# Optimization experiments

Hardware: AMD Instinct MI355X
Metric: run time of the kernel (lower is better)

Reference implementation:

```python
import jax, jax.numpy as jnp
import numpy as np
from jax import lax

B, S, H = 64, 128, 64
EPS = 1e-5


def _conv1d(x, w, b):
    # x: [B, Cin, S], w: [Cout, Cin, 3], padding=1
    y = lax.conv_general_dilated(x, w, window_strides=(1,), padding=[(1, 1)],
                                 dimension_numbers=("NCH", "OIH", "NCH"))
    return y + b[None, :, None]


def _bn(x, g, b, m, v):
    # eval-mode BatchNorm1d over channel dim of [B, C, S]
    inv = g / jnp.sqrt(v + EPS)
    return x * inv[None, :, None] + (b - m * inv)[None, :, None]


def setup_inputs() -> dict:
    key = jax.random.key(0)
    ks = jax.random.split(key, 24)
    d = {}
    d["x"] = jax.random.normal(ks[0], (B, S, 1), dtype=jnp.float32)
    sc = 0.1
    d["conv1_w"] = jax.random.normal(ks[1], (H, 1, 3), dtype=jnp.float32) * sc
    d["conv1_b"] = jax.random.normal(ks[2], (H,), dtype=jnp.float32) * sc
    d["bn1_g"] = jax.random.uniform(ks[3], (H,), dtype=jnp.float32) + 0.5
    d["bn1_b"] = jax.random.normal(ks[4], (H,), dtype=jnp.float32) * sc
    d["bn1_m"] = jax.random.normal(ks[5], (H,), dtype=jnp.float32) * sc
    d["bn1_v"] = jax.random.uniform(ks[6], (H,), dtype=jnp.float32) + 0.5
    d["conv2_w"] = jax.random.normal(ks[7], (H, H, 3), dtype=jnp.float32) * 0.05
    d["conv2_b"] = jax.random.normal(ks[8], (H,), dtype=jnp.float32) * sc
    d["bn2_g"] = jax.random.uniform(ks[9], (H,), dtype=jnp.float32) + 0.5
    d["bn2_b"] = jax.random.normal(ks[10], (H,), dtype=jnp.float32) * sc
    d["bn2_m"] = jax.random.normal(ks[11], (H,), dtype=jnp.float32) * sc
    d["bn2_v"] = jax.random.uniform(ks[12], (H,), dtype=jnp.float32) + 0.5
    d["gat_W"] = jax.random.normal(ks[13], (H, H), dtype=jnp.float32) * 0.05
    d["gat_Wb"] = jax.random.normal(ks[14], (H,), dtype=jnp.float32) * sc
    d["gat_a1"] = jax.random.normal(ks[15], (H,), dtype=jnp.float32) * sc
    d["gat_a2"] = jax.random.normal(ks[16], (H,), dtype=jnp.float32) * sc
    d["gat_ab"] = jax.random.normal(ks[17], (), dtype=jnp.float32) * sc
    d["ta_W"] = jax.random.normal(ks[18], (H, H), dtype=jnp.float32) * 0.05
    d["ta_b"] = jax.random.normal(ks[19], (H,), dtype=jnp.float32) * sc
    d["p1_W"] = jax.random.normal(ks[20], (32, H), dtype=jnp.float32) * sc
    d["p1_b"] = jax.random.normal(ks[21], (32,), dtype=jnp.float32) * sc
    d["p2_W"] = jax.random.normal(ks[22], (1, 32), dtype=jnp.float32) * sc
    d["p2_b"] = jax.random.normal(ks[23], (1,), dtype=jnp.float32) * sc
    return d


def reference(x, conv1_w, conv1_b, bn1_g, bn1_b, bn1_m, bn1_v,
              conv2_w, conv2_b, bn2_g, bn2_b, bn2_m, bn2_v,
              gat_W, gat_Wb, gat_a1, gat_a2, gat_ab,
              ta_W, ta_b, p1_W, p1_b, p2_W, p2_b):
    b, s, _ = x.shape
    # feature extraction: [B, 1, S] -> [B, H, S]
    h = jnp.transpose(x, (0, 2, 1))
    h = jax.nn.relu(_bn(_conv1d(h, conv1_w, conv1_b), bn1_g, bn1_b, bn1_m, bn1_v))
    h = jax.nn.relu(_bn(_conv1d(h, conv2_w, conv2_b), bn2_g, bn2_b, bn2_m, bn2_v))
    # flatten to N = B*S nodes of dim H
    xf = jnp.transpose(h, (0, 2, 1)).reshape(b * s, H)  # [N, H]
    # dense adjacency: softmax(xf xf^T) over rows (single chunk since B<=100)
    adj = jax.nn.softmax(xf @ xf.T, axis=1)  # [N, N]
    # GAT layer; pairwise score decomposed: a([Wh_i;Wh_j]) = Wh_i.a1 + Wh_j.a2 + b
    Wh = xf @ gat_W.T + gat_Wb  # [N, H]
    s1 = Wh @ gat_a1  # [N]
    s2 = Wh @ gat_a2  # [N]
    e = jax.nn.leaky_relu(s1[:, None] + s2[None, :] + gat_ab, 0.2)  # [N, N]
    e = jnp.where(adj > 0, e, jnp.float32(-9e15))
    att = jax.nn.softmax(e, axis=1)
    hp = att @ Wh  # [N, H]
    h2 = hp.reshape(b, s, H)
    # time attention over feature dim
    tw = jax.nn.softmax(h2 @ ta_W.T + ta_b, axis=2)
    h2 = h2 * tw
    # global average pool over sequence
    pooled = jnp.mean(h2, axis=1)  # [B, H]
    out = jax.nn.relu(pooled @ p1_W.T + p1_b) @ p2_W.T + p2_b  # [B, 1]
    return out
```

## Files before the change

### kernel.cpp

```cpp
#include <hip/hip_runtime.h>
#include <hip/hip_bf16.h>

#define Hd 64
#define Sd 128
#define Bd 64
#define Nn 8192
#define EPSd 1e-5f

__device__ __forceinline__ float wred_sum(float v) {
    for (int m = 32; m; m >>= 1) v += __shfl_xor(v, m);
    return v;
}
__device__ __forceinline__ float wred_max(float v) {
    for (int m = 32; m; m >>= 1) v = fmaxf(v, __shfl_xor(v, m));
    return v;
}
__device__ __forceinline__ float wscan_incl(float x, int lane) {
    #pragma unroll
    for (int d = 1; d < 64; d <<= 1) {
        float t = __shfl_up(x, d);
        if (lane >= d) x += t;
    }
    return x;
}

__global__ __launch_bounds__(256) void kA_feat_wh(
        const float* __restrict__ x,
        const float* __restrict__ c1w, const float* __restrict__ c1b,
        const float* __restrict__ b1g, const float* __restrict__ b1b,
        const float* __restrict__ b1m, const float* __restrict__ b1v,
        const float* __restrict__ c2w, const float* __restrict__ c2b,
        const float* __restrict__ b2g, const float* __restrict__ b2b,
        const float* __restrict__ b2m, const float* __restrict__ b2v,
        const float* __restrict__ gW, const float* __restrict__ gWb,
        const float* __restrict__ a1, const float* __restrict__ a2,
        float* __restrict__ Wh, float* __restrict__ s1, float* __restrict__ s2) {
    __shared__ float buf[14464];
    float* h1  = buf;
    float* wtk = buf + 2176;
    int b  = blockIdx.x >> 2;
    int s0 = (blockIdx.x & 3) * 32;
    int tid = threadIdx.x;
    for (int idx = tid; idx < 12288; idx += 256) {
        int j    = idx & 3;
        int c    = (idx >> 2) & 63;
        int cin4 = (idx >> 8) & 15;
        int k    = idx >> 12;
        wtk[idx] = c2w[(c * 64 + cin4 * 4 + j) * 3 + k];
    }
    for (int idx = tid; idx < 34 * 64; idx += 256) {
        int cin = idx & 63;
        int col = idx >> 6;
        int s   = s0 - 1 + col;
        float v = 0.f;
        if (s >= 0 && s < Sd) {
            float xm = (s > 0)      ? x[b * Sd + s - 1] : 0.f;
            float x0 = x[b * Sd + s];
            float xp = (s < Sd - 1) ? x[b * Sd + s + 1] : 0.f;
            float y  = c1w[cin * 3 + 0] * xm + c1w[cin * 3 + 1] * x0 + c1w[cin * 3 + 2] * xp + c1b[cin];
            float inv = b1g[cin] * rsqrtf(b1v[cin] + EPSd);
            v = fmaxf(y * inv + (b1b[cin] - b1m[cin] * inv), 0.f);
        }
        h1[col * 64 + cin] = v;
    }
    __syncthreads();
    int c = tid & 63, g = tid >> 6;
    float inv2 = b2g[c] * rsqrtf(b2v[c] + EPSd);
    float sh2  = b2b[c] - b2m[c] * inv2;
    float acc[8];
    #pragma unroll
    for (int p = 0; p < 8; ++p) acc[p] = c2b[c];
    {
        const float4* h14 = (const float4*)h1;
        const float4* wt4 = (const float4*)wtk;
        for (int cin4 = 0; cin4 < 16; ++cin4) {
            float4 xs[10];
            #pragma unroll
            for (int q = 0; q < 10; ++q) xs[q] = h14[(g * 8 + q) * 16 + cin4];
            #pragma unroll
            for (int k = 0; k < 3; ++k) {
                float4 w4 = wt4[(k * 16 + cin4) * 64 + c];
                #pragma unroll
                for (int p = 0; p < 8; ++p) {
                    float4 x4 = xs[p + k];
                    acc[p] += w4.x * x4.x + w4.y * x4.y + w4.z * x4.z + w4.w * x4.w;
                }
            }
        }
    }
    __syncthreads();
    float*  xfl  = buf;
    float4* gWT4 = (float4*)(buf + 2176);
    #pragma unroll
    for (int p = 0; p < 8; ++p)
        xfl[(g * 8 + p) * 64 + c] = fmaxf(acc[p] * inv2 + sh2, 0.f);
    for (int fidx = tid; fidx < 1024; fidx += 256) {
        int h_ = fidx >> 4, kk4 = fidx & 15;
        gWT4[kk4 * 64 + h_] = ((const float4*)gW)[fidx];
    }
    __syncthreads();
    int h = tid & 63, w = tid >> 6;
    float4 wreg[16];
    #pragma unroll
    for (int kk4 = 0; kk4 < 16; ++kk4) wreg[kk4] = gWT4[kk4 * 64 + h];
    float va1 = a1[h], va2 = a2[h], bias = gWb[h];
    const float4* xf4 = (const float4*)xfl;
    int n0 = b * Sd + s0;
    for (int q = 0; q < 8; ++q) {
        int sl = w * 8 + q;
        float accw = bias;
        #pragma unroll
        for (int kk4 = 0; kk4 < 16; ++kk4) {
            float4 x4 = xf4[sl * 16 + kk4];
            accw += wreg[kk4].x * x4.x + wreg[kk4].y * x4.y + wreg[kk4].z * x4.z + wreg[kk4].w * x4.w;
        }
        int n = n0 + sl;
        Wh[n * 64 + h] = accw;
        float r1 = wred_sum(accw * va1);
        float r2 = wred_sum(accw * va2);
        if (h == 0) { s1[n] = r1; s2[n] = r2; }
    }
}

__global__ __launch_bounds__(256) void kB_rank(
        const float* __restrict__ s2, const float* __restrict__ s1,
        const float* __restrict__ gab,
        int* __restrict__ rankPart, int* __restrict__ kPart,
        float* __restrict__ pmax) {
    __shared__ float4 ts4[64];
    int bid = blockIdx.x;
    int jg = bid >> 5, part = bid & 31;
    int tid = threadIdx.x;
    if (tid < 64) ts4[tid] = ((const float4*)(s2 + part * 256))[tid];
    __syncthreads();
    if (jg == 0 && tid < 64) {
        float4 t4 = ts4[tid];
        float m = fmaxf(fmaxf(t4.x, t4.y), fmaxf(t4.z, t4.w));
        m = wred_max(m);
        if (tid == 0) pmax[part] = m;
    }
    int j = jg * 256 + tid;
    float tj = s2[j];
    float negc = -(s1[j] + gab[0]);
    int jloc = j - part * 256;
    int cntR = 0, cntK = 0;
    #pragma unroll 4
    for (int q = 0; q < 64; ++q) {
        float4 t4 = ts4[q];
        int rb = q * 4;
        cntR += (t4.x < tj || (t4.x == tj && rb     < jloc)) ? 1 : 0;
        cntR += (t4.y < tj || (t4.y == tj && rb + 1 < jloc)) ? 1 : 0;
        cntR += (t4.z < tj || (t4.z == tj && rb + 2 < jloc)) ? 1 : 0;
        cntR += (t4.w < tj || (t4.w == tj && rb + 3 < jloc)) ? 1 : 0;
        cntK += (t4.x <= negc) ? 1 : 0;
        cntK += (t4.y <= negc) ? 1 : 0;
        cntK += (t4.z <= negc) ? 1 : 0;
        cntK += (t4.w <= negc) ? 1 : 0;
    }
    rankPart[part * 8192 + j] = cntR;
    kPart[part * 8192 + j]    = cntK;
}

__global__ __launch_bounds__(256) void kC_scatter(
        const float* __restrict__ Wh, const float* __restrict__ s2,
        const int* __restrict__ rankPart, const int* __restrict__ kPart,
        float* __restrict__ Rpos, float* __restrict__ Rneg,
        float* __restrict__ spos, float* __restrict__ sneg,
        int* __restrict__ kk) {
    __shared__ int rsl[512], ksl[512];
    __shared__ int rsum[16], ksum[16];
    int tid = threadIdx.x;
    int j0 = blockIdx.x * 16;
    for (int idx = tid; idx < 512; idx += 256) {
        int p = idx >> 4, jj = idx & 15;
        rsl[idx] = rankPart[p * 8192 + j0 + jj];
        ksl[idx] = kPart[p * 8192 + j0 + jj];
    }
    __syncthreads();
    if (tid < 16) {
        int a = 0, bq = 0;
        #pragma unroll
        for (int p = 0; p < 32; ++p) { a += rsl[p * 16 + tid]; bq += ksl[p * 16 + tid]; }
        rsum[tid] = a; ksum[tid] = bq;
    }
    __syncthreads();
    int jj = tid >> 4, h4 = tid & 15;
    int j = j0 + jj;
    int r = rsum[jj];
    float t = s2[j];
    float e1 = expf(t), e2 = expf(0.2f * t);
    float4 wv = ((const float4*)Wh)[j * 16 + h4];
    ((float4*)Rpos)[r * 16 + h4] = make_float4(e1 * wv.x, e1 * wv.y, e1 * wv.z, e1 * wv.w);
    ((float4*)Rneg)[r * 16 + h4] = make_float4(e2 * wv.x, e2 * wv.y, e2 * wv.z, e2 * wv.w);
    if (h4 == 0) { spos[r] = e1; sneg[r] = e2; kk[j] = ksum[jj]; }
}

__global__ __launch_bounds__(256) void kD_csum(
        const float* __restrict__ Rpos, const float* __restrict__ Rneg,
        const float* __restrict__ spos, const float* __restrict__ sneg,
        float* __restrict__ csP, float* __restrict__ csN,
        float* __restrict__ csp, float* __restrict__ csn) {
    __shared__ float ldsP[4][64], ldsN[4][64];
    int ch = blockIdx.x, tid = threadIdx.x;
    int h = tid & 63, w = tid >> 6;
    int rb = ch * 128 + w * 32;
    double aP = 0.0, aN = 0.0;
    #pragma unroll
    for (int r = 0; r < 32; ++r) {
        aP += Rpos[(rb + r) * 64 + h];
        aN += Rneg[(rb + r) * 64 + h];
    }
    ldsP[w][h] = (float)aP; ldsN[w][h] = (float)aN;
    __syncthreads();
    if (w == 0) {
        csP[ch * 64 + h] = ldsP[0][h] + ldsP[1][h] + ldsP[2][h] + ldsP[3][h];
    } else if (w == 1) {
        csN[ch * 64 + h] = ldsN[0][h] + ldsN[1][h] + ldsN[2][h] + ldsN[3][h];
    } else if (w == 2) {
        float v = spos[ch * 128 + h] + spos[ch * 128 + 64 + h];
        v = wred_sum(v);
        if (h == 0) csp[ch] = v;
    } else {
        float v = sneg[ch * 128 + h] + sneg[ch * 128 + 64 + h];
        v = wred_sum(v);
        if (h == 0) csn[ch] = v;
    }
}

__global__ __launch_bounds__(256) void kE_expand(
        const float* __restrict__ Rpos, const float* __restrict__ Rneg,
        const float* __restrict__ spos, const float* __restrict__ sneg,
        const float* __restrict__ csP, const float* __restrict__ csN,
        const float* __restrict__ csp, const float* __restrict__ csn,
        float* __restrict__ Ppos, float* __restrict__ Pneg,
        float* __restrict__ ppos, float* __restrict__ pneg) {
    __shared__ float ldsA[4][64], ldsB[4][64];
    __shared__ float cbPs[64], cbNs[64];
    int ch = blockIdx.x, tid = threadIdx.x;
    int h = tid & 63, w = tid >> 6;
    double bp = 0.0, bn = 0.0;
    for (int p = w; p < ch; p += 4) { bp += csP[p * 64 + h]; bn += csN[p * 64 + h]; }
    ldsA[w][h] = (float)bp; ldsB[w][h] = (float)bn;
    __syncthreads();
    if (w == 0) {
        cbPs[h] = ldsA[0][h] + ldsA[1][h] + ldsA[2][h] + ldsA[3][h];
        cbNs[h] = ldsB[0][h] + ldsB[1][h] + ldsB[2][h] + ldsB[3][h];
    }
    __syncthreads();
    float cbP = cbPs[h], cbN = cbNs[h];
    int rb = ch * 128 + w * 32;
    float v[32];
    #pragma unroll
    for (int r = 0; r < 32; ++r) v[r] = Rpos[(rb + r) * 64 + h];
    double acc = 0.0;
    #pragma unroll
    for (int r = 0; r < 32; ++r) acc += v[r];
    ldsA[w][h] = (float)acc;
    __syncthreads();
    float off = cbP;
    #pragma unroll
    for (int w2 = 0; w2 < 4; ++w2) if (w2 < w) off += ldsA[w2][h];
    double a2_ = 0.0;
    #pragma unroll
    for (int r = 0; r < 32; ++r) { Ppos[(rb + r) * 64 + h] = off + (float)a2_; a2_ += v[r]; }
    if (ch == 63 && w == 3) Ppos[Nn * 64 + h] = off + (float)a2_;
    __syncthreads();
    #pragma unroll
    for (int r = 0; r < 32; ++r) v[r] = Rneg[(rb + r) * 64 + h];
    acc = 0.0;
    #pragma unroll
    for (int r = 0; r < 32; ++r) acc += v[r];
    ldsB[w][h] = (float)acc;
    __syncthreads();
    off = cbN;
    #pragma unroll
    for (int w2 = 0; w2 < 4; ++w2) if (w2 < w) off += ldsB[w2][h];
    a2_ = 0.0;
    #pragma unroll
    for (int r = 0; r < 32; ++r) { Pneg[(rb + r) * 64 + h] = off + (float)a2_; a2_ += v[r]; }
    if (ch == 63 && w == 3) Pneg[Nn * 64 + h] = off + (float)a2_;
    if (w == 0) {
        int lane = h;
        float bs = (lane < ch) ? csp[lane] : 0.f;
        bs = wred_sum(bs);
        float v0 = spos[ch * 128 + lane], v1 = spos[ch * 128 + 64 + lane];
        float i0 = wscan_incl(v0, lane);
        float t0 = __shfl(i0, 63);
        float i1 = wscan_incl(v1, lane);
        ppos[ch * 128 + lane]      = bs + i0 - v0;
        ppos[ch * 128 + 64 + lane] = bs + t0 + i1 - v1;
        if (ch == 63 && lane == 63) ppos[Nn] = bs + t0 + i1;
    } else if (w == 1) {
        int lane = h;
        float bs = (lane < ch) ? csn[lane] : 0.f;
        bs = wred_sum(bs);
        float v0 = sneg[ch * 128 + lane], v1 = sneg[ch * 128 + 64 + lane];
        float i0 = wscan_incl(v0, lane);
        float t0 = __shfl(i0, 63);
        float i1 = wscan_incl(v1, lane);
        pneg[ch * 128 + lane]      = bs + i0 - v0;
        pneg[ch * 128 + 64 + lane] = bs + t0 + i1 - v1;
        if (ch == 63 && lane == 63) pneg[Nn] = bs + t0 + i1;
    }
}

__global__ __launch_bounds__(256) void kF_node(
        const float* __restrict__ s1, const int* __restrict__ kk,
        const float* __restrict__ pmax, const float* __restrict__ gab,
        const float* __restrict__ Ppos, const float* __restrict__ Pneg,
        const float* __restrict__ ppos, const float* __restrict__ pneg,
        const float* __restrict__ taW, const float* __restrict__ tab,
        float* __restrict__ h2) {
    __shared__ float4 wt4[1024];
    __shared__ float hl[16 * 64];
    int tid = threadIdx.x;
    for (int fidx = tid; fidx < 1024; fidx += 256) {
        int h_ = fidx >> 4, kk4 = fidx & 15;
        wt4[kk4 * 64 + h_] = ((const float4*)taW)[fidx];
    }
    float tmx = pmax[tid & 31];
    tmx = wred_max(tmx);
    __syncthreads();
    int h = tid & 63, w = tid >> 6;
    float gabv = gab[0];
    float tabv = tab[h];
    float Tp  = Ppos[Nn * 64 + h];
    float ppT = ppos[Nn];
    for (int r = 0; r < 4; ++r) {
        int n = blockIdx.x * 16 + w * 4 + r;
        float c = s1[n] + gabv;
        int k = kk[n];
        float z = c + tmx;
        float m = (z >= 0.f) ? z : 0.2f * z;
        float E1 = expf(c - m), E2 = expf(0.2f * c - m);
        float Pp = Ppos[k * 64 + h], Pn = Pneg[k * 64 + h];
        float num = E1 * (Tp - Pp) + E2 * Pn;
        float den = E1 * (ppT - ppos[k]) + E2 * pneg[k];
        float hp = num / den;
        int slot = w * 4 + r;
        hl[slot * 64 + h] = hp;
        float vv = tabv;
        const float4* hlr = (const float4*)&hl[slot * 64];
        #pragma unroll
        for (int kk4 = 0; kk4 < 16; ++kk4) {
            float4 w4 = wt4[kk4 * 64 + h];
            float4 x4 = hlr[kk4];
            vv += w4.x * x4.x + w4.y * x4.y + w4.z * x4.z + w4.w * x4.w;
        }
        float mx = wred_max(vv);
        float e = expf(vv - mx);
        float se = wred_sum(e);
        h2[n * 64 + h] = hp * (e / se);
    }
}

__global__ __launch_bounds__(256) void kG_pool(
        const float* __restrict__ h2,
        const float* __restrict__ p1W, const float* __restrict__ p1b,
        const float* __restrict__ p2W, const float* __restrict__ p2b,
        float* __restrict__ out) {
    __shared__ float pacc[4 * 64];
    __shared__ float pl[64];
    __shared__ float p1s[32 * 65];
    int tid = threadIdx.x, b = blockIdx.x;
    int w = tid >> 6, h = tid & 63;
    for (int idx = tid; idx < 2048; idx += 256) {
        int q = idx >> 6, kq = idx & 63;
        p1s[q * 65 + kq] = p1W[idx];
    }
    float a = 0.f;
    for (int s = w * 32; s < w * 32 + 32; ++s) a += h2[(b * Sd + s) * 64 + h];
    pacc[w * 64 + h] = a;
    __syncthreads();
    if (w == 0) {
        float pooled = (pacc[h] + pacc[64 + h] + pacc[128 + h] + pacc[192 + h]) * (1.f / 128.f);
        pl[h] = pooled;
        float val = 0.f;
        if (h < 32) {
            float acc = p1b[h];
            #pragma unroll
            for (int kq = 0; kq < 64; ++kq) acc += p1s[h * 65 + kq] * pl[kq];
            val = p2W[h] * fmaxf(acc, 0.f);
        }
        val = wred_sum(val);
        if (h == 0) out[b] = val + p2b[0];
    }
}

extern "C" void kernel_launch(void* const* d_in, const int* in_sizes, int n_in,
                              void* d_out, int out_size, void* d_ws, size_t ws_size,
                              hipStream_t stream) {
    const float* x    = (const float*)d_in[0];
    const float* c1w  = (const float*)d_in[1];
    const float* c1b  = (const float*)d_in[2];
    const float* b1g  = (const float*)d_in[3];
    const float* b1b  = (const float*)d_in[4];
    const float* b1m  = (const float*)d_in[5];
    const float* b1v  = (const float*)d_in[6];
    const float* c2w  = (const float*)d_in[7];
    const float* c2b  = (const float*)d_in[8];
    const float* b2g  = (const float*)d_in[9];
    const float* b2b  = (const float*)d_in[10];
    const float* b2m  = (const float*)d_in[11];
    const float* b2v  = (const float*)d_in[12];
    const float* gW   = (const float*)d_in[13];
    const float* gWb  = (const float*)d_in[14];
    const float* ga1  = (const float*)d_in[15];
    const float* ga2  = (const float*)d_in[16];
    const float* gab  = (const float*)d_in[17];
    const float* taW  = (const float*)d_in[18];
    const float* tab  = (const float*)d_in[19];
    const float* p1W  = (const float*)d_in[20];
    const float* p1b  = (const float*)d_in[21];
    const float* p2W  = (const float*)d_in[22];
    const float* p2b  = (const float*)d_in[23];
    float* out = (float*)d_out;

    float* ws = (float*)d_ws;
    float* Wh      = ws;
    float* s1      = Wh + 524288;
    float* s2v     = s1 + 8192;
    float* spos    = s2v + 8192;
    float* sneg    = spos + 8192;
    float* ppos    = sneg + 8192;
    float* pneg    = ppos + 8256;
    float* csP     = pneg + 8256;
    float* csN     = csP + 4096;
    float* csp     = csN + 4096;
    float* csn     = csp + 64;
    float* pmax    = csn + 64;
    int*   kk      = (int*)(pmax + 64);
    int*   rankPart= kk + 8192;
    int*   kPart   = rankPart + 262144;
    float* Rpos    = (float*)(kPart + 262144);
    float* Rneg    = Rpos + 524288;
    float* Ppos    = Rneg + 524288;
    float* Pneg    = Ppos + 524352;
    float* h2      = Rpos;

    kA_feat_wh<<<256, 256, 0, stream>>>(x, c1w, c1b, b1g, b1b, b1m, b1v,
                                        c2w, c2b, b2g, b2b, b2m, b2v,
                                        gW, gWb, ga1, ga2, Wh, s1, s2v);
    kB_rank<<<1024, 256, 0, stream>>>(s2v, s1, gab, rankPart, kPart, pmax);
    kC_scatter<<<512, 256, 0, stream>>>(Wh, s2v, rankPart, kPart,
                                        Rpos, Rneg, spos, sneg, kk);
    kD_csum<<<64, 256, 0, stream>>>(Rpos, Rneg, spos, sneg, csP, csN, csp, csn);
    kE_expand<<<64, 256, 0, stream>>>(Rpos, Rneg, spos, sneg, csP, csN, csp, csn,
                                      Ppos, Pneg, ppos, pneg);
    kF_node<<<512, 256, 0, stream>>>(s1, kk, pmax, gab, Ppos, Pneg, ppos, pneg,
                                     taW, tab, h2);
    kG_pool<<<64, 256, 0, stream>>>(h2, p1W, p1b, p2W, p2b, out);
}
```

Measured before the change: 68.57 us.

## Fuse scatter/cumsum/expand and node/pool kernels with inter-block flag barriers

```diff
diff --git a/kernel.cpp b/kernel.cpp
--- a/kernel.cpp
+++ b/kernel.cpp
@@ -35,11 +35,11 @@
         const float* __restrict__ gW, const float* __restrict__ gWb,
         const float* __restrict__ a1, const float* __restrict__ a2,
         float* __restrict__ Wh, float* __restrict__ s1, float* __restrict__ s2) {
-    __shared__ float buf[14464];
+    __shared__ float buf[13440];
     float* h1  = buf;
-    float* wtk = buf + 2176;
-    int b  = blockIdx.x >> 2;
-    int s0 = (blockIdx.x & 3) * 32;
+    float* wtk = buf + 1152;
+    int b  = blockIdx.x >> 3;
+    int s0 = (blockIdx.x & 7) * 16;
     int tid = threadIdx.x;
     for (int idx = tid; idx < 12288; idx += 256) {
         int j    = idx & 3;
@@ -48,7 +48,7 @@
         int k    = idx >> 12;
         wtk[idx] = c2w[(c * 64 + cin4 * 4 + j) * 3 + k];
     }
-    for (int idx = tid; idx < 34 * 64; idx += 256) {
+    for (int idx = tid; idx < 1152; idx += 256) {
         int cin = idx & 63;
         int col = idx >> 6;
         int s   = s0 - 1 + col;
@@ -67,21 +67,21 @@
     int c = tid & 63, g = tid >> 6;
     float inv2 = b2g[c] * rsqrtf(b2v[c] + EPSd);
     float sh2  = b2b[c] - b2m[c] * inv2;
-    float acc[8];
-    #pragma unroll
-    for (int p = 0; p < 8; ++p) acc[p] = c2b[c];
+    float acc[4];
+    #pragma unroll
+    for (int p = 0; p < 4; ++p) acc[p] = c2b[c];
     {
         const float4* h14 = (const float4*)h1;
         const float4* wt4 = (const float4*)wtk;
         for (int cin4 = 0; cin4 < 16; ++cin4) {
-            float4 xs[10];
+            float4 xs[6];
             #pragma unroll
-            for (int q = 0; q < 10; ++q) xs[q] = h14[(g * 8 + q) * 16 + cin4];
+            for (int q = 0; q < 6; ++q) xs[q] = h14[(g * 4 + q) * 16 + cin4];
             #pragma unroll
             for (int k = 0; k < 3; ++k) {
                 float4 w4 = wt4[(k * 16 + cin4) * 64 + c];
                 #pragma unroll
-                for (int p = 0; p < 8; ++p) {
+                for (int p = 0; p < 4; ++p) {
                     float4 x4 = xs[p + k];
                     acc[p] += w4.x * x4.x + w4.y * x4.y + w4.z * x4.z + w4.w * x4.w;
                 }
@@ -90,10 +90,10 @@
     }
     __syncthreads();
     float*  xfl  = buf;
-    float4* gWT4 = (float4*)(buf + 2176);
-    #pragma unroll
-    for (int p = 0; p < 8; ++p)
-        xfl[(g * 8 + p) * 64 + c] = fmaxf(acc[p] * inv2 + sh2, 0.f);
+    float4* gWT4 = (float4*)(buf + 1152);
+    #pragma unroll
+    for (int p = 0; p < 4; ++p)
+        xfl[(g * 4 + p) * 64 + c] = fmaxf(acc[p] * inv2 + sh2, 0.f);
     for (int fidx = tid; fidx < 1024; fidx += 256) {
         int h_ = fidx >> 4, kk4 = fidx & 15;
         gWT4[kk4 * 64 + h_] = ((const float4*)gW)[fidx];
@@ -106,8 +106,8 @@
     float va1 = a1[h], va2 = a2[h], bias = gWb[h];
     const float4* xf4 = (const float4*)xfl;
     int n0 = b * Sd + s0;
-    for (int q = 0; q < 8; ++q) {
-        int sl = w * 8 + q;
+    for (int q = 0; q < 4; ++q) {
+        int sl = w * 4 + q;
         float accw = bias;
         #pragma unroll
         for (int kk4 = 0; kk4 < 16; ++kk4) {
@@ -126,11 +126,14 @@
         const float* __restrict__ s2, const float* __restrict__ s1,
         const float* __restrict__ gab,
         int* __restrict__ rankPart, int* __restrict__ kPart,
-        float* __restrict__ pmax) {
+        float* __restrict__ pmax, int* __restrict__ flagsZ) {
     __shared__ float4 ts4[64];
     int bid = blockIdx.x;
     int jg = bid >> 5, part = bid & 31;
     int tid = threadIdx.x;
+    if (bid == 0) {
+        for (int i = tid; i < 640; i += 256) flagsZ[i] = 0;
+    }
     if (tid < 64) ts4[tid] = ((const float4*)(s2 + part * 256))[tid];
     __syncthreads();
     if (jg == 0 && tid < 64) {
@@ -161,83 +164,85 @@
     kPart[part * 8192 + j]    = cntK;
 }
 
-__global__ __launch_bounds__(256) void kC_scatter(
+__global__ __launch_bounds__(256) void kCDE(
         const float* __restrict__ Wh, const float* __restrict__ s2,
         const int* __restrict__ rankPart, const int* __restrict__ kPart,
         float* __restrict__ Rpos, float* __restrict__ Rneg,
         float* __restrict__ spos, float* __restrict__ sneg,
-        int* __restrict__ kk) {
-    __shared__ int rsl[512], ksl[512];
-    __shared__ int rsum[16], ksum[16];
-    int tid = threadIdx.x;
-    int j0 = blockIdx.x * 16;
-    for (int idx = tid; idx < 512; idx += 256) {
-        int p = idx >> 4, jj = idx & 15;
+        int* __restrict__ kk,
+        float* __restrict__ csP, float* __restrict__ csN,
+        float* __restrict__ csp, float* __restrict__ csn,
+        float* __restrict__ Ppos, float* __restrict__ Pneg,
+        float* __restrict__ ppos, float* __restrict__ pneg,
+        int* __restrict__ flag1, int* __restrict__ flag2) {
+    __shared__ int rsl[4096], ksl[4096];
+    __shared__ float e1s[128], e2s[128];
+    __shared__ int rj[128];
+    __shared__ float ldsA[4][64], ldsB[4][64], cbPs[64], cbNs[64];
+    int ch = blockIdx.x, tid = threadIdx.x;
+    int j0 = ch * 128;
+    for (int idx = tid; idx < 4096; idx += 256) {
+        int p = idx >> 7, jj = idx & 127;
         rsl[idx] = rankPart[p * 8192 + j0 + jj];
         ksl[idx] = kPart[p * 8192 + j0 + jj];
     }
     __syncthreads();
-    if (tid < 16) {
-        int a = 0, bq = 0;
+    if (tid < 128) {
+        int r = 0, kq = 0;
         #pragma unroll
-        for (int p = 0; p < 32; ++p) { a += rsl[p * 16 + tid]; bq += ksl[p * 16 + tid]; }
-        rsum[tid] = a; ksum[tid] = bq;
-    }
-    __syncthreads();
-    int jj = tid >> 4, h4 = tid & 15;
-    int j = j0 + jj;
-    int r = rsum[jj];
-    float t = s2[j];
-    float e1 = expf(t), e2 = expf(0.2f * t);
-    float4 wv = ((const float4*)Wh)[j * 16 + h4];
-    ((float4*)Rpos)[r * 16 + h4] = make_float4(e1 * wv.x, e1 * wv.y, e1 * wv.z, e1 * wv.w);
-    ((float4*)Rneg)[r * 16 + h4] = make_float4(e2 * wv.x, e2 * wv.y, e2 * wv.z, e2 * wv.w);
-    if (h4 == 0) { spos[r] = e1; sneg[r] = e2; kk[j] = ksum[jj]; }
-}
-
-__global__ __launch_bounds__(256) void kD_csum(
-        const float* __restrict__ Rpos, const float* __restrict__ Rneg,
-        const float* __restrict__ spos, const float* __restrict__ sneg,
-        float* __restrict__ csP, float* __restrict__ csN,
-        float* __restrict__ csp, float* __restrict__ csn) {
-    __shared__ float ldsP[4][64], ldsN[4][64];
-    int ch = blockIdx.x, tid = threadIdx.x;
+        for (int p = 0; p < 32; ++p) { r += rsl[p * 128 + tid]; kq += ksl[p * 128 + tid]; }
+        rj[tid] = r;
+        float t = s2[j0 + tid];
+        float e1 = expf(t), e2 = expf(0.2f * t);
+        e1s[tid] = e1; e2s[tid] = e2;
+        spos[r] = e1; sneg[r] = e2;
+        kk[j0 + tid] = kq;
+    }
+    __syncthreads();
+    for (int it = tid; it < 2048; it += 256) {
+        int jj = it >> 4, h4 = it & 15;
+        int r = rj[jj];
+        float4 wv = ((const float4*)Wh)[(j0 + jj) * 16 + h4];
+        float e1 = e1s[jj], e2 = e2s[jj];
+        ((float4*)Rpos)[r * 16 + h4] = make_float4(e1 * wv.x, e1 * wv.y, e1 * wv.z, e1 * wv.w);
+        ((float4*)Rneg)[r * 16 + h4] = make_float4(e2 * wv.x, e2 * wv.y, e2 * wv.z, e2 * wv.w);
+    }
+    __threadfence();
+    __syncthreads();
+    if (tid == 0) atomicExch(&flag1[ch], 1);
+    if (tid < 64) { while (atomicAdd(&flag1[tid], 0) == 0) __builtin_amdgcn_s_sleep(2); }
+    __syncthreads();
+    __threadfence();
     int h = tid & 63, w = tid >> 6;
     int rb = ch * 128 + w * 32;
-    double aP = 0.0, aN = 0.0;
-    #pragma unroll
-    for (int r = 0; r < 32; ++r) {
-        aP += Rpos[(rb + r) * 64 + h];
-        aN += Rneg[(rb + r) * 64 + h];
-    }
-    ldsP[w][h] = (float)aP; ldsN[w][h] = (float)aN;
+    float v[32], u[32];
+    #pragma unroll
+    for (int r = 0; r < 32; ++r) { v[r] = Rpos[(rb + r) * 64 + h]; u[r] = Rneg[(rb + r) * 64 + h]; }
+    double sP = 0.0, sN = 0.0;
+    #pragma unroll
+    for (int r = 0; r < 32; ++r) { sP += v[r]; sN += u[r]; }
+    float sPf = (float)sP, sNf = (float)sN;
+    ldsA[w][h] = sPf; ldsB[w][h] = sNf;
     __syncthreads();
     if (w == 0) {
-        csP[ch * 64 + h] = ldsP[0][h] + ldsP[1][h] + ldsP[2][h] + ldsP[3][h];
+        csP[ch * 64 + h] = ldsA[0][h] + ldsA[1][h] + ldsA[2][h] + ldsA[3][h];
     } else if (w == 1) {
-        csN[ch * 64 + h] = ldsN[0][h] + ldsN[1][h] + ldsN[2][h] + ldsN[3][h];
+        csN[ch * 64 + h] = ldsB[0][h] + ldsB[1][h] + ldsB[2][h] + ldsB[3][h];
     } else if (w == 2) {
-        float v = spos[ch * 128 + h] + spos[ch * 128 + 64 + h];
-        v = wred_sum(v);
-        if (h == 0) csp[ch] = v;
+        float vv = spos[ch * 128 + h] + spos[ch * 128 + 64 + h];
+        vv = wred_sum(vv);
+        if (h == 0) csp[ch] = vv;
     } else {
-        float v = sneg[ch * 128 + h] + sneg[ch * 128 + 64 + h];
-        v = wred_sum(v);
-        if (h == 0) csn[ch] = v;
-    }
-}
-
-__global__ __launch_bounds__(256) void kE_expand(
-        const float* __restrict__ Rpos, const float* __restrict__ Rneg,
-        const float* __restrict__ spos, const float* __restrict__ sneg,
-        const float* __restrict__ csP, const float* __restrict__ csN,
-        const float* __restrict__ csp, const float* __restrict__ csn,
-        float* __restrict__ Ppos, float* __restrict__ Pneg,
-        float* __restrict__ ppos, float* __restrict__ pneg) {
-    __shared__ float ldsA[4][64], ldsB[4][64];
-    __shared__ float cbPs[64], cbNs[64];
-    int ch = blockIdx.x, tid = threadIdx.x;
-    int h = tid & 63, w = tid >> 6;
+        float vv = sneg[ch * 128 + h] + sneg[ch * 128 + 64 + h];
+        vv = wred_sum(vv);
+        if (h == 0) csn[ch] = vv;
+    }
+    __threadfence();
+    __syncthreads();
+    if (tid == 0) atomicExch(&flag2[ch], 1);
+    if (tid < 64) { while (atomicAdd(&flag2[tid], 0) == 0) __builtin_amdgcn_s_sleep(2); }
+    __syncthreads();
+    __threadfence();
     double bp = 0.0, bn = 0.0;
     for (int p = w; p < ch; p += 4) { bp += csP[p * 64 + h]; bn += csN[p * 64 + h]; }
     ldsA[w][h] = (float)bp; ldsB[w][h] = (float)bn;
@@ -247,38 +252,19 @@
         cbNs[h] = ldsB[0][h] + ldsB[1][h] + ldsB[2][h] + ldsB[3][h];
     }
     __syncthreads();
-    float cbP = cbPs[h], cbN = cbNs[h];
-    int rb = ch * 128 + w * 32;
-    float v[32];
-    #pragma unroll
-    for (int r = 0; r < 32; ++r) v[r] = Rpos[(rb + r) * 64 + h];
-    double acc = 0.0;
-    #pragma unroll
-    for (int r = 0; r < 32; ++r) acc += v[r];
-    ldsA[w][h] = (float)acc;
-    __syncthreads();
-    float off = cbP;
-    #pragma unroll
-    for (int w2 = 0; w2 < 4; ++w2) if (w2 < w) off += ldsA[w2][h];
-    double a2_ = 0.0;
-    #pragma unroll
-    for (int r = 0; r < 32; ++r) { Ppos[(rb + r) * 64 + h] = off + (float)a2_; a2_ += v[r]; }
-    if (ch == 63 && w == 3) Ppos[Nn * 64 + h] = off + (float)a2_;
-    __syncthreads();
-    #pragma unroll
-    for (int r = 0; r < 32; ++r) v[r] = Rneg[(rb + r) * 64 + h];
-    acc = 0.0;
-    #pragma unroll
-    for (int r = 0; r < 32; ++r) acc += v[r];
-    ldsB[w][h] = (float)acc;
-    __syncthreads();
-    off = cbN;
-    #pragma unroll
-    for (int w2 = 0; w2 < 4; ++w2) if (w2 < w) off += ldsB[w2][h];
-    a2_ = 0.0;
-    #pragma unroll
-    for (int r = 0; r < 32; ++r) { Pneg[(rb + r) * 64 + h] = off + (float)a2_; a2_ += v[r]; }
-    if (ch == 63 && w == 3) Pneg[Nn * 64 + h] = off + (float)a2_;
+    ldsA[w][h] = sPf; ldsB[w][h] = sNf;
+    __syncthreads();
+    float offP = cbPs[h], offN = cbNs[h];
+    #pragma unroll
+    for (int w2 = 0; w2 < 4; ++w2) if (w2 < w) { offP += ldsA[w2][h]; offN += ldsB[w2][h]; }
+    double a = 0.0;
+    #pragma unroll
+    for (int r = 0; r < 32; ++r) { Ppos[(rb + r) * 64 + h] = offP + (float)a; a += v[r]; }
+    if (ch == 63 && w == 3) Ppos[Nn * 64 + h] = offP + (float)a;
+    a = 0.0;
+    #pragma unroll
+    for (int r = 0; r < 32; ++r) { Pneg[(rb + r) * 64 + h] = offN + (float)a; a += u[r]; }
+    if (ch == 63 && w == 3) Pneg[Nn * 64 + h] = offN + (float)a;
     if (w == 0) {
         int lane = h;
         float bs = (lane < ch) ? csp[lane] : 0.f;
@@ -304,16 +290,22 @@
     }
 }
 
-__global__ __launch_bounds__(256) void kF_node(
+__global__ __launch_bounds__(256) void kFG(
         const float* __restrict__ s1, const int* __restrict__ kk,
         const float* __restrict__ pmax, const float* __restrict__ gab,
         const float* __restrict__ Ppos, const float* __restrict__ Pneg,
         const float* __restrict__ ppos, const float* __restrict__ pneg,
         const float* __restrict__ taW, const float* __restrict__ tab,
-        float* __restrict__ h2) {
+        const float* __restrict__ p1W, const float* __restrict__ p1b,
+        const float* __restrict__ p2W, const float* __restrict__ p2b,
+        float* __restrict__ h2, float* __restrict__ out,
+        int* __restrict__ flagF) {
     __shared__ float4 wt4[1024];
     __shared__ float hl[16 * 64];
-    int tid = threadIdx.x;
+    __shared__ float pacc[4 * 64];
+    __shared__ float pl[64];
+    __shared__ float p1s[32 * 65];
+    int tid = threadIdx.x, bid = blockIdx.x;
     for (int fidx = tid; fidx < 1024; fidx += 256) {
         int h_ = fidx >> 4, kk4 = fidx & 15;
         wt4[kk4 * 64 + h_] = ((const float4*)taW)[fidx];
@@ -327,7 +319,7 @@
     float Tp  = Ppos[Nn * 64 + h];
     float ppT = ppos[Nn];
     for (int r = 0; r < 4; ++r) {
-        int n = blockIdx.x * 16 + w * 4 + r;
+        int n = bid * 16 + w * 4 + r;
         float c = s1[n] + gabv;
         int k = kk[n];
         float z = c + tmx;
@@ -352,18 +344,14 @@
         float se = wred_sum(e);
         h2[n * 64 + h] = hp * (e / se);
     }
-}
-
-__global__ __launch_bounds__(256) void kG_pool(
-        const float* __restrict__ h2,
-        const float* __restrict__ p1W, const float* __restrict__ p1b,
-        const float* __restrict__ p2W, const float* __restrict__ p2b,
-        float* __restrict__ out) {
-    __shared__ float pacc[4 * 64];
-    __shared__ float pl[64];
-    __shared__ float p1s[32 * 65];
-    int tid = threadIdx.x, b = blockIdx.x;
-    int w = tid >> 6, h = tid & 63;
+    __threadfence();
+    __syncthreads();
+    if (tid == 0) atomicExch(&flagF[bid], 1);
+    if (bid & 7) return;
+    int b = bid >> 3;
+    if (tid < 8) { while (atomicAdd(&flagF[bid + tid], 0) == 0) __builtin_amdgcn_s_sleep(2); }
+    __syncthreads();
+    __threadfence();
     for (int idx = tid; idx < 2048; idx += 256) {
         int q = idx >> 6, kq = idx & 63;
         p1s[q * 65 + kq] = p1W[idx];
@@ -429,7 +417,11 @@
     float* csp     = csN + 4096;
     float* csn     = csp + 64;
     float* pmax    = csn + 64;
-    int*   kk      = (int*)(pmax + 64);
+    int*   flags   = (int*)(pmax + 64);
+    int*   flag1   = flags;
+    int*   flag2   = flags + 64;
+    int*   flagF   = flags + 128;
+    int*   kk      = flags + 640;
     int*   rankPart= kk + 8192;
     int*   kPart   = rankPart + 262144;
     float* Rpos    = (float*)(kPart + 262144);
@@ -438,16 +430,14 @@
     float* Pneg    = Ppos + 524352;
     float* h2      = Rpos;
 
-    kA_feat_wh<<<256, 256, 0, stream>>>(x, c1w, c1b, b1g, b1b, b1m, b1v,
+    kA_feat_wh<<<512, 256, 0, stream>>>(x, c1w, c1b, b1g, b1b, b1m, b1v,
                                         c2w, c2b, b2g, b2b, b2m, b2v,
                                         gW, gWb, ga1, ga2, Wh, s1, s2v);
-    kB_rank<<<1024, 256, 0, stream>>>(s2v, s1, gab, rankPart, kPart, pmax);
-    kC_scatter<<<512, 256, 0, stream>>>(Wh, s2v, rankPart, kPart,
-                                        Rpos, Rneg, spos, sneg, kk);
-    kD_csum<<<64, 256, 0, stream>>>(Rpos, Rneg, spos, sneg, csP, csN, csp, csn);
-    kE_expand<<<64, 256, 0, stream>>>(Rpos, Rneg, spos, sneg, csP, csN, csp, csn,
-                                      Ppos, Pneg, ppos, pneg);
-    kF_node<<<512, 256, 0, stream>>>(s1, kk, pmax, gab, Ppos, Pneg, ppos, pneg,
-                                     taW, tab, h2);
-    kG_pool<<<64, 256, 0, stream>>>(h2, p1W, p1b, p2W, p2b, out);
-}
+    kB_rank<<<1024, 256, 0, stream>>>(s2v, s1, gab, rankPart, kPart, pmax, flags);
+    kCDE<<<64, 256, 0, stream>>>(Wh, s2v, rankPart, kPart,
+                                 Rpos, Rneg, spos, sneg, kk,
+                                 csP, csN, csp, csn,
+                                 Ppos, Pneg, ppos, pneg, flag1, flag2);
+    kFG<<<512, 256, 0, stream>>>(s1, kk, pmax, gab, Ppos, Pneg, ppos, pneg,
+                                 taW, tab, p1W, p1b, p2W, p2b, h2, out, flagF);
+}
```

New measurement: 166.4 us. 2.43x slower.

## Scatter sorted indices instead of rows and fuse chunk sums with local prefix scans

Applied to the files above, without the earlier changes.

```diff
diff --git a/kernel.cpp b/kernel.cpp
--- a/kernel.cpp
+++ b/kernel.cpp
@@ -42,11 +42,12 @@
     int s0 = (blockIdx.x & 3) * 32;
     int tid = threadIdx.x;
     for (int idx = tid; idx < 12288; idx += 256) {
-        int j    = idx & 3;
-        int c    = (idx >> 2) & 63;
-        int cin4 = (idx >> 8) & 15;
-        int k    = idx >> 12;
-        wtk[idx] = c2w[(c * 64 + cin4 * 4 + j) * 3 + k];
+        int c   = idx / 192;
+        int rem = idx - c * 192;
+        int cin = rem / 3;
+        int k   = rem - cin * 3;
+        int cin4 = cin >> 2, j = cin & 3;
+        wtk[(k * 16 + cin4) * 256 + c * 4 + j] = c2w[idx];
     }
     for (int idx = tid; idx < 34 * 64; idx += 256) {
         int cin = idx & 63;
@@ -162,180 +163,166 @@
 }
 
 __global__ __launch_bounds__(256) void kC_scatter(
-        const float* __restrict__ Wh, const float* __restrict__ s2,
+        const float* __restrict__ s2,
         const int* __restrict__ rankPart, const int* __restrict__ kPart,
-        float* __restrict__ Rpos, float* __restrict__ Rneg,
-        float* __restrict__ spos, float* __restrict__ sneg,
+        int* __restrict__ jsorted, float* __restrict__ e1so, float* __restrict__ e2so,
         int* __restrict__ kk) {
-    __shared__ int rsl[512], ksl[512];
-    __shared__ int rsum[16], ksum[16];
-    int tid = threadIdx.x;
-    int j0 = blockIdx.x * 16;
-    for (int idx = tid; idx < 512; idx += 256) {
-        int p = idx >> 4, jj = idx & 15;
-        rsl[idx] = rankPart[p * 8192 + j0 + jj];
-        ksl[idx] = kPart[p * 8192 + j0 + jj];
-    }
-    __syncthreads();
-    if (tid < 16) {
-        int a = 0, bq = 0;
-        #pragma unroll
-        for (int p = 0; p < 32; ++p) { a += rsl[p * 16 + tid]; bq += ksl[p * 16 + tid]; }
-        rsum[tid] = a; ksum[tid] = bq;
-    }
-    __syncthreads();
-    int jj = tid >> 4, h4 = tid & 15;
-    int j = j0 + jj;
-    int r = rsum[jj];
+    int j = blockIdx.x * 256 + threadIdx.x;
+    int r = 0, kq = 0;
+    #pragma unroll
+    for (int p = 0; p < 32; ++p) { r += rankPart[p * 8192 + j]; kq += kPart[p * 8192 + j]; }
     float t = s2[j];
-    float e1 = expf(t), e2 = expf(0.2f * t);
-    float4 wv = ((const float4*)Wh)[j * 16 + h4];
-    ((float4*)Rpos)[r * 16 + h4] = make_float4(e1 * wv.x, e1 * wv.y, e1 * wv.z, e1 * wv.w);
-    ((float4*)Rneg)[r * 16 + h4] = make_float4(e2 * wv.x, e2 * wv.y, e2 * wv.z, e2 * wv.w);
-    if (h4 == 0) { spos[r] = e1; sneg[r] = e2; kk[j] = ksum[jj]; }
-}
-
-__global__ __launch_bounds__(256) void kD_csum(
-        const float* __restrict__ Rpos, const float* __restrict__ Rneg,
-        const float* __restrict__ spos, const float* __restrict__ sneg,
+    jsorted[r] = j;
+    e1so[r] = expf(t);
+    e2so[r] = expf(0.2f * t);
+    kk[j] = kq;
+}
+
+__global__ __launch_bounds__(256) void kD_dual(
+        const float* __restrict__ Wh, const int* __restrict__ jsorted,
+        const float* __restrict__ e1so, const float* __restrict__ e2so,
         float* __restrict__ csP, float* __restrict__ csN,
-        float* __restrict__ csp, float* __restrict__ csn) {
-    __shared__ float ldsP[4][64], ldsN[4][64];
-    int ch = blockIdx.x, tid = threadIdx.x;
+        float* __restrict__ csp, float* __restrict__ csn,
+        float* __restrict__ PLpos, float* __restrict__ PLneg,
+        float* __restrict__ pLp, float* __restrict__ pLn) {
+    __shared__ float ldsA[4][64], ldsB[4][64];
+    int bid = blockIdx.x, tid = threadIdx.x;
     int h = tid & 63, w = tid >> 6;
-    int rb = ch * 128 + w * 32;
-    double aP = 0.0, aN = 0.0;
-    #pragma unroll
-    for (int r = 0; r < 32; ++r) {
-        aP += Rpos[(rb + r) * 64 + h];
-        aN += Rneg[(rb + r) * 64 + h];
-    }
-    ldsP[w][h] = (float)aP; ldsN[w][h] = (float)aN;
-    __syncthreads();
-    if (w == 0) {
-        csP[ch * 64 + h] = ldsP[0][h] + ldsP[1][h] + ldsP[2][h] + ldsP[3][h];
-    } else if (w == 1) {
-        csN[ch * 64 + h] = ldsN[0][h] + ldsN[1][h] + ldsN[2][h] + ldsN[3][h];
-    } else if (w == 2) {
-        float v = spos[ch * 128 + h] + spos[ch * 128 + 64 + h];
-        v = wred_sum(v);
-        if (h == 0) csp[ch] = v;
+    if (bid < 64) {
+        int ch = bid;
+        int rb = ch * 128 + w * 32;
+        double aP = 0.0, aN = 0.0;
+        #pragma unroll
+        for (int r = 0; r < 32; ++r) {
+            int j = jsorted[rb + r];
+            float wv = Wh[j * 64 + h];
+            aP += e1so[rb + r] * wv;
+            aN += e2so[rb + r] * wv;
+        }
+        ldsA[w][h] = (float)aP; ldsB[w][h] = (float)aN;
+        __syncthreads();
+        if (w == 0) {
+            csP[ch * 64 + h] = ldsA[0][h] + ldsA[1][h] + ldsA[2][h] + ldsA[3][h];
+        } else if (w == 1) {
+            csN[ch * 64 + h] = ldsB[0][h] + ldsB[1][h] + ldsB[2][h] + ldsB[3][h];
+        } else if (w == 2) {
+            float vv = e1so[ch * 128 + h] + e1so[ch * 128 + 64 + h];
+            vv = wred_sum(vv);
+            if (h == 0) csp[ch] = vv;
+        } else {
+            float vv = e2so[ch * 128 + h] + e2so[ch * 128 + 64 + h];
+            vv = wred_sum(vv);
+            if (h == 0) csn[ch] = vv;
+        }
     } else {
-        float v = sneg[ch * 128 + h] + sneg[ch * 128 + 64 + h];
-        v = wred_sum(v);
-        if (h == 0) csn[ch] = v;
-    }
-}
-
-__global__ __launch_bounds__(256) void kE_expand(
-        const float* __restrict__ Rpos, const float* __restrict__ Rneg,
-        const float* __restrict__ spos, const float* __restrict__ sneg,
-        const float* __restrict__ csP, const float* __restrict__ csN,
-        const float* __restrict__ csp, const float* __restrict__ csn,
-        float* __restrict__ Ppos, float* __restrict__ Pneg,
-        float* __restrict__ ppos, float* __restrict__ pneg) {
-    __shared__ float ldsA[4][64], ldsB[4][64];
-    __shared__ float cbPs[64], cbNs[64];
-    int ch = blockIdx.x, tid = threadIdx.x;
-    int h = tid & 63, w = tid >> 6;
-    double bp = 0.0, bn = 0.0;
-    for (int p = w; p < ch; p += 4) { bp += csP[p * 64 + h]; bn += csN[p * 64 + h]; }
-    ldsA[w][h] = (float)bp; ldsB[w][h] = (float)bn;
-    __syncthreads();
-    if (w == 0) {
-        cbPs[h] = ldsA[0][h] + ldsA[1][h] + ldsA[2][h] + ldsA[3][h];
-        cbNs[h] = ldsB[0][h] + ldsB[1][h] + ldsB[2][h] + ldsB[3][h];
-    }
-    __syncthreads();
-    float cbP = cbPs[h], cbN = cbNs[h];
-    int rb = ch * 128 + w * 32;
-    float v[32];
-    #pragma unroll
-    for (int r = 0; r < 32; ++r) v[r] = Rpos[(rb + r) * 64 + h];
-    double acc = 0.0;
-    #pragma unroll
-    for (int r = 0; r < 32; ++r) acc += v[r];
-    ldsA[w][h] = (float)acc;
-    __syncthreads();
-    float off = cbP;
-    #pragma unroll
-    for (int w2 = 0; w2 < 4; ++w2) if (w2 < w) off += ldsA[w2][h];
-    double a2_ = 0.0;
-    #pragma unroll
-    for (int r = 0; r < 32; ++r) { Ppos[(rb + r) * 64 + h] = off + (float)a2_; a2_ += v[r]; }
-    if (ch == 63 && w == 3) Ppos[Nn * 64 + h] = off + (float)a2_;
-    __syncthreads();
-    #pragma unroll
-    for (int r = 0; r < 32; ++r) v[r] = Rneg[(rb + r) * 64 + h];
-    acc = 0.0;
-    #pragma unroll
-    for (int r = 0; r < 32; ++r) acc += v[r];
-    ldsB[w][h] = (float)acc;
-    __syncthreads();
-    off = cbN;
-    #pragma unroll
-    for (int w2 = 0; w2 < 4; ++w2) if (w2 < w) off += ldsB[w2][h];
-    a2_ = 0.0;
-    #pragma unroll
-    for (int r = 0; r < 32; ++r) { Pneg[(rb + r) * 64 + h] = off + (float)a2_; a2_ += v[r]; }
-    if (ch == 63 && w == 3) Pneg[Nn * 64 + h] = off + (float)a2_;
-    if (w == 0) {
-        int lane = h;
-        float bs = (lane < ch) ? csp[lane] : 0.f;
-        bs = wred_sum(bs);
-        float v0 = spos[ch * 128 + lane], v1 = spos[ch * 128 + 64 + lane];
-        float i0 = wscan_incl(v0, lane);
-        float t0 = __shfl(i0, 63);
-        float i1 = wscan_incl(v1, lane);
-        ppos[ch * 128 + lane]      = bs + i0 - v0;
-        ppos[ch * 128 + 64 + lane] = bs + t0 + i1 - v1;
-        if (ch == 63 && lane == 63) ppos[Nn] = bs + t0 + i1;
-    } else if (w == 1) {
-        int lane = h;
-        float bs = (lane < ch) ? csn[lane] : 0.f;
-        bs = wred_sum(bs);
-        float v0 = sneg[ch * 128 + lane], v1 = sneg[ch * 128 + 64 + lane];
-        float i0 = wscan_incl(v0, lane);
-        float t0 = __shfl(i0, 63);
-        float i1 = wscan_incl(v1, lane);
-        pneg[ch * 128 + lane]      = bs + i0 - v0;
-        pneg[ch * 128 + 64 + lane] = bs + t0 + i1 - v1;
-        if (ch == 63 && lane == 63) pneg[Nn] = bs + t0 + i1;
+        int ch = bid - 64;
+        int rb = ch * 128 + w * 32;
+        float v[32], u[32];
+        #pragma unroll
+        for (int r = 0; r < 32; ++r) {
+            int j = jsorted[rb + r];
+            float wv = Wh[j * 64 + h];
+            v[r] = e1so[rb + r] * wv;
+            u[r] = e2so[rb + r] * wv;
+        }
+        double sP = 0.0, sN = 0.0;
+        #pragma unroll
+        for (int r = 0; r < 32; ++r) { sP += v[r]; sN += u[r]; }
+        ldsA[w][h] = (float)sP; ldsB[w][h] = (float)sN;
+        __syncthreads();
+        float offP = 0.f, offN = 0.f;
+        #pragma unroll
+        for (int w2 = 0; w2 < 4; ++w2) if (w2 < w) { offP += ldsA[w2][h]; offN += ldsB[w2][h]; }
+        double a = 0.0;
+        #pragma unroll
+        for (int r = 0; r < 32; ++r) { PLpos[(rb + r) * 64 + h] = offP + (float)a; a += v[r]; }
+        a = 0.0;
+        #pragma unroll
+        for (int r = 0; r < 32; ++r) { PLneg[(rb + r) * 64 + h] = offN + (float)a; a += u[r]; }
+        if (w == 0) {
+            int lane = h;
+            float v0 = e1so[ch * 128 + lane], v1 = e1so[ch * 128 + 64 + lane];
+            float i0 = wscan_incl(v0, lane);
+            float t0 = __shfl(i0, 63);
+            float i1 = wscan_incl(v1, lane);
+            pLp[ch * 128 + lane]      = i0 - v0;
+            pLp[ch * 128 + 64 + lane] = t0 + i1 - v1;
+        } else if (w == 1) {
+            int lane = h;
+            float v0 = e2so[ch * 128 + lane], v1 = e2so[ch * 128 + 64 + lane];
+            float i0 = wscan_incl(v0, lane);
+            float t0 = __shfl(i0, 63);
+            float i1 = wscan_incl(v1, lane);
+            pLn[ch * 128 + lane]      = i0 - v0;
+            pLn[ch * 128 + 64 + lane] = t0 + i1 - v1;
+        }
     }
 }
 
 __global__ __launch_bounds__(256) void kF_node(
         const float* __restrict__ s1, const int* __restrict__ kk,
         const float* __restrict__ pmax, const float* __restrict__ gab,
-        const float* __restrict__ Ppos, const float* __restrict__ Pneg,
-        const float* __restrict__ ppos, const float* __restrict__ pneg,
+        const float* __restrict__ PLpos, const float* __restrict__ PLneg,
+        const float* __restrict__ pLp, const float* __restrict__ pLn,
+        const float* __restrict__ csP, const float* __restrict__ csN,
+        const float* __restrict__ csp, const float* __restrict__ csn,
         const float* __restrict__ taW, const float* __restrict__ tab,
         float* __restrict__ h2) {
     __shared__ float4 wt4[1024];
     __shared__ float hl[16 * 64];
+    __shared__ float cpP[65 * 64], cpN[65 * 64];
+    __shared__ float cpp[65], cpn[65];
     int tid = threadIdx.x;
+    int h = tid & 63, w = tid >> 6;
     for (int fidx = tid; fidx < 1024; fidx += 256) {
         int h_ = fidx >> 4, kk4 = fidx & 15;
         wt4[kk4 * 64 + h_] = ((const float4*)taW)[fidx];
     }
+    if (w == 0) {
+        double a = 0.0;
+        for (int ch = 0; ch < 64; ++ch) { cpP[ch * 64 + h] = (float)a; a += csP[ch * 64 + h]; }
+        cpP[64 * 64 + h] = (float)a;
+    } else if (w == 1) {
+        double a = 0.0;
+        for (int ch = 0; ch < 64; ++ch) { cpN[ch * 64 + h] = (float)a; a += csN[ch * 64 + h]; }
+        cpN[64 * 64 + h] = (float)a;
+    } else if (w == 2) {
+        float v = csp[h];
+        float i = wscan_incl(v, h);
+        cpp[h] = i - v;
+        if (h == 63) cpp[64] = i;
+    } else {
+        float v = csn[h];
+        float i = wscan_incl(v, h);
+        cpn[h] = i - v;
+        if (h == 63) cpn[64] = i;
+    }
     float tmx = pmax[tid & 31];
     tmx = wred_max(tmx);
     __syncthreads();
-    int h = tid & 63, w = tid >> 6;
     float gabv = gab[0];
     float tabv = tab[h];
-    float Tp  = Ppos[Nn * 64 + h];
-    float ppT = ppos[Nn];
+    float Tp  = cpP[64 * 64 + h];
+    float ppT = cpp[64];
     for (int r = 0; r < 4; ++r) {
         int n = blockIdx.x * 16 + w * 4 + r;
         float c = s1[n] + gabv;
         int k = kk[n];
+        int ch = k >> 7;
+        float PLpv = 0.f, PLnv = 0.f, pLpv = 0.f, pLnv = 0.f;
+        if (k < Nn) {
+            PLpv = PLpos[k * 64 + h]; PLnv = PLneg[k * 64 + h];
+            pLpv = pLp[k];            pLnv = pLn[k];
+        }
+        float Pp = cpP[ch * 64 + h] + PLpv;
+        float Pn = cpN[ch * 64 + h] + PLnv;
+        float qp = cpp[ch] + pLpv;
+        float qn = cpn[ch] + pLnv;
         float z = c + tmx;
         float m = (z >= 0.f) ? z : 0.2f * z;
         float E1 = expf(c - m), E2 = expf(0.2f * c - m);
-        float Pp = Ppos[k * 64 + h], Pn = Pneg[k * 64 + h];
         float num = E1 * (Tp - Pp) + E2 * Pn;
-        float den = E1 * (ppT - ppos[k]) + E2 * pneg[k];
+        float den = E1 * (ppT - qp) + E2 * qn;
         float hp = num / den;
         int slot = w * 4 + r;
         hl[slot * 64 + h] = hp;
@@ -420,34 +407,31 @@
     float* Wh      = ws;
     float* s1      = Wh + 524288;
     float* s2v     = s1 + 8192;
-    float* spos    = s2v + 8192;
-    float* sneg    = spos + 8192;
-    float* ppos    = sneg + 8192;
-    float* pneg    = ppos + 8256;
-    float* csP     = pneg + 8256;
+    float* e1so    = s2v + 8192;
+    float* e2so    = e1so + 8192;
+    float* csP     = e2so + 8192;
     float* csN     = csP + 4096;
     float* csp     = csN + 4096;
     float* csn     = csp + 64;
     float* pmax    = csn + 64;
-    int*   kk      = (int*)(pmax + 64);
+    float* pLp     = pmax + 64;
+    float* pLn     = pLp + 8192;
+    float* PLpos   = pLn + 8192;
+    float* PLneg   = PLpos + 524288;
+    int*   jsorted = (int*)(PLneg + 524288);
+    int*   kk      = jsorted + 8192;
     int*   rankPart= kk + 8192;
     int*   kPart   = rankPart + 262144;
-    float* Rpos    = (float*)(kPart + 262144);
-    float* Rneg    = Rpos + 524288;
-    float* Ppos    = Rneg + 524288;
-    float* Pneg    = Ppos + 524352;
-    float* h2      = Rpos;
+    float* h2      = (float*)rankPart;
 
     kA_feat_wh<<<256, 256, 0, stream>>>(x, c1w, c1b, b1g, b1b, b1m, b1v,
                                         c2w, c2b, b2g, b2b, b2m, b2v,
                                         gW, gWb, ga1, ga2, Wh, s1, s2v);
     kB_rank<<<1024, 256, 0, stream>>>(s2v, s1, gab, rankPart, kPart, pmax);
-    kC_scatter<<<512, 256, 0, stream>>>(Wh, s2v, rankPart, kPart,
-                                        Rpos, Rneg, spos, sneg, kk);
-    kD_csum<<<64, 256, 0, stream>>>(Rpos, Rneg, spos, sneg, csP, csN, csp, csn);
-    kE_expand<<<64, 256, 0, stream>>>(Rpos, Rneg, spos, sneg, csP, csN, csp, csn,
-                                      Ppos, Pneg, ppos, pneg);
-    kF_node<<<512, 256, 0, stream>>>(s1, kk, pmax, gab, Ppos, Pneg, ppos, pneg,
-                                     taW, tab, h2);
+    kC_scatter<<<32, 256, 0, stream>>>(s2v, rankPart, kPart, jsorted, e1so, e2so, kk);
+    kD_dual<<<128, 256, 0, stream>>>(Wh, jsorted, e1so, e2so, csP, csN, csp, csn,
+                                     PLpos, PLneg, pLp, pLn);
+    kF_node<<<512, 256, 0, stream>>>(s1, kk, pmax, gab, PLpos, PLneg, pLp, pLn,
+                                     csP, csN, csp, csn, taW, tab, h2);
     kG_pool<<<64, 256, 0, stream>>>(h2, p1W, p1b, p2W, p2b, out);
 }
```

After: 58.86 us, median of 2. -14.2%, faster.
